# Kernel optimization log

Hardware: AMD Instinct MI355X
Metric: run time of the kernel (lower is better)

Reference implementation:

```python
import jax, jax.numpy as jnp
import numpy as np

N = 100000
E = 3200000
IN_DIM = 256
HID = 64
OUT = 40


def setup_inputs() -> dict:
    key = jax.random.key(0)
    ks = jax.random.split(key, 8)
    x = jax.random.normal(ks[0], (N, IN_DIM), dtype=jnp.float32)
    edge_index = jax.random.randint(ks[1], (2, E), 0, N, dtype=jnp.int64)
    # Glorot-ish init for weights
    W1 = jax.random.normal(ks[2], (IN_DIM, HID), dtype=jnp.float32) / np.sqrt(IN_DIM)
    b1 = jnp.zeros((HID,), dtype=jnp.float32)
    W2 = jax.random.normal(ks[3], (HID, HID), dtype=jnp.float32) / np.sqrt(HID)
    b2 = jnp.zeros((HID,), dtype=jnp.float32)
    W3 = jax.random.normal(ks[4], (HID, OUT), dtype=jnp.float32) / np.sqrt(HID)
    b3 = jax.random.normal(ks[5], (OUT,), dtype=jnp.float32) * 0.01
    return {"x": x, "edge_index": edge_index,
            "W1": W1, "b1": b1, "W2": W2, "b2": b2, "W3": W3, "b3": b3}


def _gcn_norm(edge_index, n):
    # Add self-loops, compute symmetric normalization deg^-1/2 A deg^-1/2
    loop = jnp.arange(n, dtype=edge_index.dtype)
    src = jnp.concatenate([edge_index[0], loop])
    dst = jnp.concatenate([edge_index[1], loop])
    deg = jax.ops.segment_sum(jnp.ones_like(dst, dtype=jnp.float32), dst,
                              num_segments=n)
    dinv = jnp.where(deg > 0, jax.lax.rsqrt(deg), 0.0)
    norm = dinv[src] * dinv[dst]  # [E+N]
    return src, dst, norm


def _gcn_conv(x, src, dst, norm, W, b, n):
    h = x @ W                                  # transform first (small dim)
    msg = h[src] * norm[:, None]               # gather + scale
    out = jax.ops.segment_sum(msg, dst, num_segments=n)  # scatter-add
    return out + b


def reference(x, edge_index, W1, b1, W2, b2, W3, b3):
    n = x.shape[0]
    src, dst, norm = _gcn_norm(edge_index, n)
    h = jax.nn.relu(_gcn_conv(x, src, dst, norm, W1, b1, n))
    h = jax.nn.relu(_gcn_conv(h, src, dst, norm, W2, b2, n))
    logits = h @ W3 + b3
    return jax.nn.log_softmax(logits, axis=1)
```

## Files before the change

kernel.cpp:

```cpp
#include <hip/hip_runtime.h>
#include <hip/hip_fp16.h>
#include <cstdint>


constexpr int CHUNK = 8192;
constexpr int BKCAP = 8192;

typedef __attribute__((ext_vector_type(8))) short bf16x8;
typedef __attribute__((ext_vector_type(4))) float f32x4;

__device__ __forceinline__ int cvt2bf(float a, float b) {
    int r;
    asm("v_cvt_pk_bf16_f32 %0, %1, %2" : "=v"(r) : "v"(a), "v"(b));
    return r;
}
__device__ __forceinline__ unsigned short bf16_1(float a) {
    return (unsigned short)(cvt2bf(a, a) & 0xFFFF);
}

__global__ __launch_bounds__(256) void p2_localsort(
        const int* __restrict__ esrc, const int* __restrict__ edst, int E,
        unsigned* __restrict__ pairs1, int* __restrict__ cntMat,
        int* __restrict__ startMat, int NBK) {
    __shared__ int hist[1024];
    __shared__ int wsum[256];
    __shared__ unsigned lp[CHUNK];
    const int t = threadIdx.x, blk = blockIdx.x;
    const int base = blk * CHUNK;
    const int cnt = min(CHUNK, E - base);
    for (int i = t; i < 1024; i += 256) hist[i] = 0;
    __syncthreads();
    for (int i = t; i < cnt; i += 256) atomicAdd(&hist[edst[base + i] >> 7], 1);
    __syncthreads();
    int h0 = hist[4*t], h1 = hist[4*t+1], h2 = hist[4*t+2], h3 = hist[4*t+3];
    int s = h0 + h1 + h2 + h3;
    wsum[t] = s; __syncthreads();
    #pragma unroll
    for (int o = 1; o < 256; o <<= 1) {
        int x = (t >= o) ? wsum[t - o] : 0;
        __syncthreads(); wsum[t] += x; __syncthreads();
    }
    int run = wsum[t] - s;
    int e0 = run, e1 = run + h0, e2 = e1 + h1, e3 = e2 + h2;
    hist[4*t] = e0; hist[4*t+1] = e1; hist[4*t+2] = e2; hist[4*t+3] = e3;
    if (4*t     < NBK) { cntMat[(size_t)blk*NBK + 4*t]     = h0; startMat[(size_t)blk*NBK + 4*t]     = e0; }
    if (4*t + 1 < NBK) { cntMat[(size_t)blk*NBK + 4*t + 1] = h1; startMat[(size_t)blk*NBK + 4*t + 1] = e1; }
    if (4*t + 2 < NBK) { cntMat[(size_t)blk*NBK + 4*t + 2] = h2; startMat[(size_t)blk*NBK + 4*t + 2] = e2; }
    if (4*t + 3 < NBK) { cntMat[(size_t)blk*NBK + 4*t + 3] = h3; startMat[(size_t)blk*NBK + 4*t + 3] = e3; }
    __syncthreads();
    for (int i = t; i < cnt; i += 256) {
        int d = edst[base + i];
        int pos = atomicAdd(&hist[d >> 7], 1);
        lp[pos] = ((unsigned)(d & 127) << 17) | (unsigned)esrc[base + i];
    }
    __syncthreads();
    for (int i = t; i < cnt; i += 256) pairs1[base + i] = lp[i];
}

__global__ __launch_bounds__(256) void p3_colscan(int* __restrict__ cntMat,
        int* __restrict__ TB, int nchunks, int NBK) {
    __shared__ int buf[512];
    const int t = threadIdx.x, b = blockIdx.x;
    int v0 = (t < nchunks) ? cntMat[(size_t)t*NBK + b] : 0;
    int v1 = (t + 256 < nchunks) ? cntMat[(size_t)(t + 256)*NBK + b] : 0;
    buf[t] = v0; buf[t + 256] = v1; __syncthreads();
    #pragma unroll
    for (int o = 1; o < 512; o <<= 1) {
        int x0 = (t >= o) ? buf[t - o] : 0;
        int x1 = (t + 256 >= o) ? buf[t + 256 - o] : 0;
        __syncthreads(); buf[t] += x0; buf[t + 256] += x1; __syncthreads();
    }
    if (t < nchunks) cntMat[(size_t)t*NBK + b] = buf[t] - v0;
    if (t + 256 < nchunks) cntMat[(size_t)(t + 256)*NBK + b] = buf[t + 256] - v1;
    if (t == 0) TB[b] = buf[511];
}

__global__ __launch_bounds__(256) void p4_scan(const int* __restrict__ TB,
        int* __restrict__ bucketBase, int NBK, int E) {
    __shared__ int buf[1024];
    __shared__ int wsum[256];
    const int t = threadIdx.x;
    for (int i = t; i < 1024; i += 256) buf[i] = (i < NBK) ? TB[i] : 0;
    __syncthreads();
    int h0 = buf[4*t], h1 = buf[4*t+1], h2 = buf[4*t+2], h3 = buf[4*t+3];
    int s = h0 + h1 + h2 + h3;
    wsum[t] = s; __syncthreads();
    #pragma unroll
    for (int o = 1; o < 256; o <<= 1) {
        int x = (t >= o) ? wsum[t - o] : 0;
        __syncthreads(); wsum[t] += x; __syncthreads();
    }
    int run = wsum[t] - s;
    int e0 = run, e1 = run + h0, e2 = e1 + h1, e3 = e2 + h2;
    if (4*t     < NBK) bucketBase[4*t]     = e0;
    if (4*t + 1 < NBK) bucketBase[4*t + 1] = e1;
    if (4*t + 2 < NBK) bucketBase[4*t + 2] = e2;
    if (4*t + 3 < NBK) bucketBase[4*t + 3] = e3;
    if (t == 0) bucketBase[NBK] = E;
}

__global__ __launch_bounds__(256) void p6_sortcsr(
        const unsigned* __restrict__ pairs1, const int* __restrict__ cumMat,
        const int* __restrict__ startMat, const int* __restrict__ TB,
        const int* __restrict__ bucketBase, int nchunks, int NBK,
        int* __restrict__ csrc, int* __restrict__ rofs,
        float* __restrict__ dinv, int N, int E) {
    __shared__ unsigned lp[BKCAP];
    __shared__ int ccum[512];
    __shared__ int cstart[512];
    __shared__ int hist[128];
    __shared__ int sc[128];
    __shared__ int foffs[128];
    const int t = threadIdx.x, b = blockIdx.x;
    const int total0 = TB[b];
    const int total = min(total0, BKCAP);
    const int base = bucketBase[b];
    for (int i = t; i < nchunks; i += 256) {
        ccum[i]   = cumMat[(size_t)i * NBK + b];
        cstart[i] = startMat[(size_t)i * NBK + b];
    }
    if (t < 128) hist[t] = 0;
    if (t == 0) ccum[nchunks] = total0;
    __syncthreads();
    for (int i = t; i < total; i += 256) {
        int lo = 0, hi = nchunks - 1;
        while (lo < hi) {
            int mid = (lo + hi + 1) >> 1;
            if (ccum[mid] <= i) lo = mid; else hi = mid - 1;
        }
        unsigned v = pairs1[(size_t)lo * CHUNK + cstart[lo] + (i - ccum[lo])];
        lp[i] = v;
        atomicAdd(&hist[v >> 17], 1);
    }
    __syncthreads();
    if (t < 128) sc[t] = hist[t];
    __syncthreads();
    #pragma unroll
    for (int o = 1; o < 128; o <<= 1) {
        int x = (t >= o && t < 128) ? sc[t - o] : 0;
        __syncthreads();
        if (t < 128) sc[t] += x;
        __syncthreads();
    }
    if (t < 128) {
        int excl = sc[t] - hist[t];
        foffs[t] = excl;
        int node = b * 128 + t;
        if (node < N) {
            rofs[node] = base + excl;
            dinv[node] = rsqrtf((float)hist[t] + 1.0f);
        }
    }
    if (b == 0 && t == 255) rofs[N] = E;
    __syncthreads();
    for (int i = t; i < total; i += 256) {
        unsigned v = lp[i];
        int pos = atomicAdd(&foffs[v >> 17], 1);
        csrc[base + pos] = (int)(v & 0x1FFFFu);
    }
}

template<int K>
__global__ __launch_bounds__(256) void k_gemm(const float* __restrict__ X,
        const float* __restrict__ Wm, const float* __restrict__ dinv,
        __half* __restrict__ G, int nrows) {
    constexpr int BK = 32;
    constexpr int NCH = K / BK;
    constexpr int XP = 68;
    __shared__ float Xs[BK * XP];
    __shared__ float Ws[BK * 64];
    const int t = threadIdx.x;
    const int cg = t & 15;
    const int rg = t >> 4;
    const int brow = blockIdx.x * 64;

    float acc[4][4];
    #pragma unroll
    for (int r = 0; r < 4; ++r)
        #pragma unroll
        for (int c = 0; c < 4; ++c) acc[r][c] = 0.f;

    for (int ch = 0; ch < NCH; ++ch) {
        if (ch) __syncthreads();
        #pragma unroll
        for (int i = 0; i < 2; ++i) {
            int f = t + i * 256;
            int r = f >> 3, c4 = f & 7;
            int gr = brow + r;
            float4 v = make_float4(0.f, 0.f, 0.f, 0.f);
            if (gr < nrows)
                v = *(const float4*)(X + (size_t)gr * K + ch * BK + c4 * 4);
            int rsw = r ^ (c4 << 2);
            Xs[(c4 * 4 + 0) * XP + rsw] = v.x;
            Xs[(c4 * 4 + 1) * XP + rsw] = v.y;
            Xs[(c4 * 4 + 2) * XP + rsw] = v.z;
            Xs[(c4 * 4 + 3) * XP + rsw] = v.w;
        }
        #pragma unroll
        for (int i = 0; i < 2; ++i) {
            int f = t + i * 256;
            int k = f >> 4, c4 = f & 15;
            *(float4*)(Ws + k * 64 + c4 * 4) =
                *(const float4*)(Wm + (size_t)(ch * BK + k) * 64 + c4 * 4);
        }
        __syncthreads();

        #pragma unroll
        for (int k = 0; k < BK; ++k) {
            const int xsw = (k >> 2) << 2;
            float4 xa = *(const float4*)(Xs + k * XP + ((rg * 4) ^ xsw));
            float4 wv = *(const float4*)(Ws + k * 64 + cg * 4);
            acc[0][0] += xa.x * wv.x; acc[0][1] += xa.x * wv.y;
            acc[0][2] += xa.x * wv.z; acc[0][3] += xa.x * wv.w;
            acc[1][0] += xa.y * wv.x; acc[1][1] += xa.y * wv.y;
            acc[1][2] += xa.y * wv.z; acc[1][3] += xa.y * wv.w;
            acc[2][0] += xa.z * wv.x; acc[2][1] += xa.z * wv.y;
            acc[2][2] += xa.z * wv.z; acc[2][3] += xa.z * wv.w;
            acc[3][0] += xa.w * wv.x; acc[3][1] += xa.w * wv.y;
            acc[3][2] += xa.w * wv.z; acc[3][3] += xa.w * wv.w;
        }
    }
    #pragma unroll
    for (int r = 0; r < 4; ++r) {
        int gr = brow + rg * 4 + r;
        if (gr < nrows) {
            float dv = dinv[gr];
            __half2 h01 = __floats2half2_rn(acc[r][0] * dv, acc[r][1] * dv);
            __half2 h23 = __floats2half2_rn(acc[r][2] * dv, acc[r][3] * dv);
            uint2 pk;
            pk.x = *(unsigned*)&h01; pk.y = *(unsigned*)&h23;
            *(uint2*)(G + (size_t)gr * 64 + cg * 4) = pk;
        }
    }
}

#define ACC8H(HA, V) { \
    HA[0] = __hadd2(HA[0], *(const __half2*)&(V).x); \
    HA[1] = __hadd2(HA[1], *(const __half2*)&(V).y); \
    HA[2] = __hadd2(HA[2], *(const __half2*)&(V).z); \
    HA[3] = __hadd2(HA[3], *(const __half2*)&(V).w); }

#define GATHER_REDUCE(G_, beg_, end_, g_, p_, HA) { \
    int e = (beg_) + (g_); \
    for (; e + 8 < (end_); e += 16) { \
        int s0 = csrc[e]; \
        int s1 = csrc[e + 8]; \
        uint4 v0 = *(const uint4*)((G_) + (size_t)s0 * 64 + (p_) * 8); \
        uint4 v1 = *(const uint4*)((G_) + (size_t)s1 * 64 + (p_) * 8); \
        ACC8H(HA, v0) \
        ACC8H(HA, v1) \
    } \
    if (e < (end_)) { \
        int s = csrc[e]; \
        uint4 v = *(const uint4*)((G_) + (size_t)s * 64 + (p_) * 8); \
        ACC8H(HA, v) \
    } \
    _Pragma("unroll") \
    for (int off = 8; off <= 32; off <<= 1) { \
        _Pragma("unroll") \
        for (int q = 0; q < 4; ++q) { \
            int o = __shfl_xor(*(int*)&HA[q], off); \
            HA[q] = __hadd2(HA[q], *(__half2*)&o); \
        } \
    } }

#define CONV_EPILOGUE(G_, d_, dv_, bias_, p_, HA, HOUT) { \
    uint4 sv = *(const uint4*)((G_) + (size_t)(d_) * 64 + (p_) * 8); \
    float4 bb0 = *(const float4*)((bias_) + (p_) * 8); \
    float4 bb1 = *(const float4*)((bias_) + (p_) * 8 + 4); \
    float2 a0 = __half22float2(HA[0]), a1 = __half22float2(HA[1]); \
    float2 a2 = __half22float2(HA[2]), a3 = __half22float2(HA[3]); \
    float2 s0 = __half22float2(*(const __half2*)&sv.x); \
    float2 s1 = __half22float2(*(const __half2*)&sv.y); \
    float2 s2 = __half22float2(*(const __half2*)&sv.z); \
    float2 s3 = __half22float2(*(const __half2*)&sv.w); \
    HOUT[0] = fmaxf((a0.x + s0.x) * (dv_) + bb0.x, 0.f); \
    HOUT[1] = fmaxf((a0.y + s0.y) * (dv_) + bb0.y, 0.f); \
    HOUT[2] = fmaxf((a1.x + s1.x) * (dv_) + bb0.z, 0.f); \
    HOUT[3] = fmaxf((a1.y + s1.y) * (dv_) + bb0.w, 0.f); \
    HOUT[4] = fmaxf((a2.x + s2.x) * (dv_) + bb1.x, 0.f); \
    HOUT[5] = fmaxf((a2.y + s2.y) * (dv_) + bb1.y, 0.f); \
    HOUT[6] = fmaxf((a3.x + s3.x) * (dv_) + bb1.z, 0.f); \
    HOUT[7] = fmaxf((a3.y + s3.y) * (dv_) + bb1.w, 0.f); }

__global__ __launch_bounds__(256) void k_agg_mid(const __half* __restrict__ G,
        const int* __restrict__ rofs, const int* __restrict__ csrc,
        const float* __restrict__ dinv, const float* __restrict__ b1,
        const float* __restrict__ W2, __half* __restrict__ G2, int nrows) {
    __shared__ unsigned short W2t[64 * 68];
    __shared__ unsigned short H1s[16 * 68];
    const int t = threadIdx.x;
    for (int i = t; i < 4096; i += 256) {
        int k = i >> 6, c = i & 63;
        W2t[c * 68 + k] = bf16_1(W2[i]);
    }
    const int l = t & 63;
    const int w = t >> 6;
    const int g = l >> 3, p = l & 7;
    const int nbase = blockIdx.x * 16;
    #pragma unroll 1
    for (int i = 0; i < 4; ++i) {
        int row = w * 4 + i;
        int d = nbase + row;
        if (d < nrows) {
            int beg = rofs[d], end = rofs[d + 1];
            __half2 ha[4];
            #pragma unroll
            for (int q = 0; q < 4; ++q) ha[q] = __half2(__float2half(0.f), __float2half(0.f));
            GATHER_REDUCE(G, beg, end, g, p, ha)
            float dv = dinv[d];
            float h1[8];
            CONV_EPILOGUE(G, d, dv, b1, p, ha, h1)
            if (g == 0) {
                int4 pk;
                pk.x = cvt2bf(h1[0], h1[1]); pk.y = cvt2bf(h1[2], h1[3]);
                pk.z = cvt2bf(h1[4], h1[5]); pk.w = cvt2bf(h1[6], h1[7]);
                *(int4*)(&H1s[row * 68 + p * 8]) = pk;
            }
        }
    }
    __syncthreads();
    const int c16 = l & 15, g4 = l >> 4;
    f32x4 acc = {0.f, 0.f, 0.f, 0.f};
    #pragma unroll
    for (int kc = 0; kc < 2; ++kc) {
        bf16x8 a = *(bf16x8*)(&H1s[c16 * 68 + kc * 32 + g4 * 8]);
        bf16x8 b = *(bf16x8*)(&W2t[(w * 16 + c16) * 68 + kc * 32 + g4 * 8]);
        acc = __builtin_amdgcn_mfma_f32_16x16x32_bf16(a, b, acc, 0, 0, 0);
    }
    #pragma unroll
    for (int r = 0; r < 4; ++r) {
        int d = nbase + g4 * 4 + r;
        if (d < nrows)
            G2[(size_t)d * 64 + w * 16 + c16] = __float2half(acc[r] * dinv[d]);
    }
}

__global__ __launch_bounds__(256) void k_agg_out(const __half* __restrict__ G2,
        const int* __restrict__ rofs, const int* __restrict__ csrc,
        const float* __restrict__ dinv, const float* __restrict__ b2,
        const float* __restrict__ W3, const float* __restrict__ b3,
        float* __restrict__ out, int nrows) {
    constexpr int LP = 49;
    __shared__ unsigned short W3t[48 * 68];
    __shared__ unsigned short H2s[16 * 68];
    __shared__ float Ls[16 * LP];
    __shared__ float b3s[48];
    const int t = threadIdx.x;
    for (int i = t; i < 48 * 64; i += 256) {
        int c = i >> 6, k = i & 63;
        W3t[c * 68 + k] = (c < 40) ? bf16_1(W3[k * 40 + c]) : (unsigned short)0;
    }
    if (t < 48) b3s[t] = (t < 40) ? b3[t] : 0.f;
    const int l = t & 63;
    const int w = t >> 6;
    const int g = l >> 3, p = l & 7;
    const int nbase = blockIdx.x * 16;
    #pragma unroll 1
    for (int i = 0; i < 4; ++i) {
        int row = w * 4 + i;
        int d = nbase + row;
        if (d < nrows) {
            int beg = rofs[d], end = rofs[d + 1];
            __half2 ha[4];
            #pragma unroll
            for (int q = 0; q < 4; ++q) ha[q] = __half2(__float2half(0.f), __float2half(0.f));
            GATHER_REDUCE(G2, beg, end, g, p, ha)
            float dv = dinv[d];
            float h2[8];
            CONV_EPILOGUE(G2, d, dv, b2, p, ha, h2)
            if (g == 0) {
                int4 pk;
                pk.x = cvt2bf(h2[0], h2[1]); pk.y = cvt2bf(h2[2], h2[3]);
                pk.z = cvt2bf(h2[4], h2[5]); pk.w = cvt2bf(h2[6], h2[7]);
                *(int4*)(&H2s[row * 68 + p * 8]) = pk;
            }
        }
    }
    __syncthreads();
    const int c16 = l & 15, g4 = l >> 4;
    if (w < 3) {
        f32x4 acc = {0.f, 0.f, 0.f, 0.f};
        #pragma unroll
        for (int kc = 0; kc < 2; ++kc) {
            bf16x8 a = *(bf16x8*)(&H2s[c16 * 68 + kc * 32 + g4 * 8]);
            bf16x8 b = *(bf16x8*)(&W3t[(w * 16 + c16) * 68 + kc * 32 + g4 * 8]);
            acc = __builtin_amdgcn_mfma_f32_16x16x32_bf16(a, b, acc, 0, 0, 0);
        }
        #pragma unroll
        for (int r = 0; r < 4; ++r)
            Ls[(g4 * 4 + r) * LP + w * 16 + c16] = acc[r] + b3s[w * 16 + c16];
    }
    __syncthreads();
    #pragma unroll 1
    for (int i = 0; i < 4; ++i) {
        int row = w * 4 + i;
        int d = nbase + row;
        if (d >= nrows) continue;
        float v = (l < 40) ? Ls[row * LP + l] : -3.4e38f;
        float m = v;
        #pragma unroll
        for (int off = 1; off < 64; off <<= 1) m = fmaxf(m, __shfl_xor(m, off));
        float ex = (l < 40) ? expf(v - m) : 0.f;
        float ssum = ex;
        #pragma unroll
        for (int off = 1; off < 64; off <<= 1) ssum += __shfl_xor(ssum, off);
        float lse = m + logf(ssum);
        if (l < 40) out[(size_t)d * 40 + l] = v - lse;
    }
}

extern "C" void kernel_launch(void* const* d_in, const int* in_sizes, int n_in,
                              void* d_out, int out_size, void* d_ws, size_t ws_size,
                              hipStream_t stream) {
    const float* x  = (const float*)d_in[0];
    const int*   ei = (const int*)d_in[1];
    const float* W1 = (const float*)d_in[2];
    const float* b1 = (const float*)d_in[3];
    const float* W2 = (const float*)d_in[4];
    const float* b2 = (const float*)d_in[5];
    const float* W3 = (const float*)d_in[6];
    const float* b3 = (const float*)d_in[7];
    float* out = (float*)d_out;

    const int HID = in_sizes[3];
    const int IND = in_sizes[2] / HID;
    const int N   = in_sizes[0] / IND;
    const int E   = in_sizes[1] / 2;
    (void)HID; (void)n_in; (void)out_size; (void)ws_size;

    const int NBK     = (N + 127) >> 7;
    const int nchunks = (E + CHUNK - 1) / CHUNK;

    char* ws = (char*)d_ws;
    size_t off = 0;
    auto alloc = [&](size_t bytes) -> char* {
        char* p = ws + off;
        off = (off + bytes + 255) & ~(size_t)255;
        return p;
    };
    size_t gbytes = (size_t)N * 64 * 2;
    size_t p1bytes = (size_t)E * 4;
    int*      cntMat     = (int*)     alloc((size_t)nchunks * NBK * 4);
    int*      startMat   = (int*)     alloc((size_t)nchunks * NBK * 4);
    int*      TB         = (int*)     alloc((size_t)NBK * 4);
    int*      bucketBase = (int*)     alloc(((size_t)NBK + 1) * 4);
    float*    dinv       = (float*)   alloc((size_t)N * 4);
    int*      rofs       = (int*)     alloc(((size_t)N + 1) * 4);
    int*      csrc       = (int*)     alloc((size_t)E * 4);
    __half*   g          = (__half*)  alloc(gbytes > p1bytes ? gbytes : p1bytes);
    __half*   g2         = (__half*)  alloc(gbytes);
    unsigned* pairs1     = (unsigned*)g;

    const int* esrc = ei;
    const int* edst = ei + E;
    const int gM  = (N + 63) / 64;
    const int gA  = (N + 15) / 16;

    p2_localsort<<<nchunks, 256, 0, stream>>>(esrc, edst, E, pairs1, cntMat, startMat, NBK);
    p3_colscan  <<<NBK, 256, 0, stream>>>(cntMat, TB, nchunks, NBK);
    p4_scan     <<<1, 256, 0, stream>>>(TB, bucketBase, NBK, E);
    p6_sortcsr  <<<NBK, 256, 0, stream>>>(pairs1, cntMat, startMat, TB, bucketBase,
                                          nchunks, NBK, csrc, rofs, dinv, N, E);

    k_gemm<256> <<<gM, 256, 0, stream>>>(x, W1, dinv, g, N);
    k_agg_mid   <<<gA, 256, 0, stream>>>(g, rofs, csrc, dinv, b1, W2, g2, N);
    k_agg_out   <<<gA, 256, 0, stream>>>(g2, rofs, csrc, dinv, b2, W3, b3, out, N);
}
```

Before: 300.6 us.

## Process four destination rows per wavefront concurrently in aggregation kernels

Changes the aggregation mapping so that each wavefront handles four destination rows at once, with 16 lanes per row split into two edge-slices of eight feature lanes. Before, each wavefront looped serially over its four rows with eight edge-slices per row. The gather loop is unrolled to four outstanding 16-byte loads per lane, and the cross-lane reduction shrinks to a single shuffle. The aim is more memory-level parallelism and fewer serial latency chains per row, at the cost of divergence when the four rows have uneven degrees.

New measurement: 277.0 us. 7.9% less time.

```diff
diff --git a/kernel.cpp b/kernel.cpp
--- a/kernel.cpp
+++ b/kernel.cpp
@@ -240,28 +240,25 @@
     HA[2] = __hadd2(HA[2], *(const __half2*)&(V).z); \
     HA[3] = __hadd2(HA[3], *(const __half2*)&(V).w); }
 
-#define GATHER_REDUCE(G_, beg_, end_, g_, p_, HA) { \
-    int e = (beg_) + (g_); \
-    for (; e + 8 < (end_); e += 16) { \
-        int s0 = csrc[e]; \
-        int s1 = csrc[e + 8]; \
-        uint4 v0 = *(const uint4*)((G_) + (size_t)s0 * 64 + (p_) * 8); \
-        uint4 v1 = *(const uint4*)((G_) + (size_t)s1 * 64 + (p_) * 8); \
-        ACC8H(HA, v0) \
-        ACC8H(HA, v1) \
+#define GATHER16(G_, beg_, end_, s_, p_, HA) { \
+    int e = (beg_) + (s_); \
+    for (; e + 6 < (end_); e += 8) { \
+        int i0 = csrc[e], i1 = csrc[e + 2], i2 = csrc[e + 4], i3 = csrc[e + 6]; \
+        uint4 v0 = *(const uint4*)((G_) + (size_t)i0 * 64 + (p_) * 8); \
+        uint4 v1 = *(const uint4*)((G_) + (size_t)i1 * 64 + (p_) * 8); \
+        uint4 v2 = *(const uint4*)((G_) + (size_t)i2 * 64 + (p_) * 8); \
+        uint4 v3 = *(const uint4*)((G_) + (size_t)i3 * 64 + (p_) * 8); \
+        ACC8H(HA, v0) ACC8H(HA, v1) ACC8H(HA, v2) ACC8H(HA, v3) \
     } \
-    if (e < (end_)) { \
-        int s = csrc[e]; \
-        uint4 v = *(const uint4*)((G_) + (size_t)s * 64 + (p_) * 8); \
+    for (; e < (end_); e += 2) { \
+        int ii = csrc[e]; \
+        uint4 v = *(const uint4*)((G_) + (size_t)ii * 64 + (p_) * 8); \
         ACC8H(HA, v) \
     } \
     _Pragma("unroll") \
-    for (int off = 8; off <= 32; off <<= 1) { \
-        _Pragma("unroll") \
-        for (int q = 0; q < 4; ++q) { \
-            int o = __shfl_xor(*(int*)&HA[q], off); \
-            HA[q] = __hadd2(HA[q], *(__half2*)&o); \
-        } \
+    for (int q = 0; q < 4; ++q) { \
+        int o = __shfl_xor(*(int*)&HA[q], 8); \
+        HA[q] = __hadd2(HA[q], *(__half2*)&o); \
     } }
 
 #define CONV_EPILOGUE(G_, d_, dv_, bias_, p_, HA, HOUT) { \
@@ -296,31 +293,30 @@
     }
     const int l = t & 63;
     const int w = t >> 6;
-    const int g = l >> 3, p = l & 7;
+    const int n = l >> 4;
+    const int s = (l >> 3) & 1;
+    const int p = l & 7;
+    const int row = w * 4 + n;
+    const int d = blockIdx.x * 16 + row;
+    if (d < nrows) {
+        const int beg = rofs[d], end = rofs[d + 1];
+        __half2 ha[4];
+        #pragma unroll
+        for (int q = 0; q < 4; ++q) ha[q] = __half2(__float2half(0.f), __float2half(0.f));
+        GATHER16(G, beg, end, s, p, ha)
+        float dv = dinv[d];
+        float h1[8];
+        CONV_EPILOGUE(G, d, dv, b1, p, ha, h1)
+        if (s == 0) {
+            int4 pk;
+            pk.x = cvt2bf(h1[0], h1[1]); pk.y = cvt2bf(h1[2], h1[3]);
+            pk.z = cvt2bf(h1[4], h1[5]); pk.w = cvt2bf(h1[6], h1[7]);
+            *(int4*)(&H1s[row * 68 + p * 8]) = pk;
+        }
+    }
+    __syncthreads();
+    const int c16 = l & 15, g4 = l >> 4;
     const int nbase = blockIdx.x * 16;
-    #pragma unroll 1
-    for (int i = 0; i < 4; ++i) {
-        int row = w * 4 + i;
-        int d = nbase + row;
-        if (d < nrows) {
-            int beg = rofs[d], end = rofs[d + 1];
-            __half2 ha[4];
-            #pragma unroll
-            for (int q = 0; q < 4; ++q) ha[q] = __half2(__float2half(0.f), __float2half(0.f));
-            GATHER_REDUCE(G, beg, end, g, p, ha)
-            float dv = dinv[d];
-            float h1[8];
-            CONV_EPILOGUE(G, d, dv, b1, p, ha, h1)
-            if (g == 0) {
-                int4 pk;
-                pk.x = cvt2bf(h1[0], h1[1]); pk.y = cvt2bf(h1[2], h1[3]);
-                pk.z = cvt2bf(h1[4], h1[5]); pk.w = cvt2bf(h1[6], h1[7]);
-                *(int4*)(&H1s[row * 68 + p * 8]) = pk;
-            }
-        }
-    }
-    __syncthreads();
-    const int c16 = l & 15, g4 = l >> 4;
     f32x4 acc = {0.f, 0.f, 0.f, 0.f};
     #pragma unroll
     for (int kc = 0; kc < 2; ++kc) {
@@ -330,9 +326,9 @@
     }
     #pragma unroll
     for (int r = 0; r < 4; ++r) {
-        int d = nbase + g4 * 4 + r;
-        if (d < nrows)
-            G2[(size_t)d * 64 + w * 16 + c16] = __float2half(acc[r] * dinv[d]);
+        int dd = nbase + g4 * 4 + r;
+        if (dd < nrows)
+            G2[(size_t)dd * 64 + w * 16 + c16] = __float2half(acc[r] * dinv[dd]);
     }
 }
 
@@ -354,31 +350,30 @@
     if (t < 48) b3s[t] = (t < 40) ? b3[t] : 0.f;
     const int l = t & 63;
     const int w = t >> 6;
-    const int g = l >> 3, p = l & 7;
+    const int n = l >> 4;
+    const int s = (l >> 3) & 1;
+    const int p = l & 7;
+    const int row = w * 4 + n;
+    const int d = blockIdx.x * 16 + row;
+    if (d < nrows) {
+        const int beg = rofs[d], end = rofs[d + 1];
+        __half2 ha[4];
+        #pragma unroll
+        for (int q = 0; q < 4; ++q) ha[q] = __half2(__float2half(0.f), __float2half(0.f));
+        GATHER16(G2, beg, end, s, p, ha)
+        float dv = dinv[d];
+        float h2[8];
+        CONV_EPILOGUE(G2, d, dv, b2, p, ha, h2)
+        if (s == 0) {
+            int4 pk;
+            pk.x = cvt2bf(h2[0], h2[1]); pk.y = cvt2bf(h2[2], h2[3]);
+            pk.z = cvt2bf(h2[4], h2[5]); pk.w = cvt2bf(h2[6], h2[7]);
+            *(int4*)(&H2s[row * 68 + p * 8]) = pk;
+        }
+    }
+    __syncthreads();
+    const int c16 = l & 15, g4 = l >> 4;
     const int nbase = blockIdx.x * 16;
-    #pragma unroll 1
-    for (int i = 0; i < 4; ++i) {
-        int row = w * 4 + i;
-        int d = nbase + row;
-        if (d < nrows) {
-            int beg = rofs[d], end = rofs[d + 1];
-            __half2 ha[4];
-            #pragma unroll
-            for (int q = 0; q < 4; ++q) ha[q] = __half2(__float2half(0.f), __float2half(0.f));
-            GATHER_REDUCE(G2, beg, end, g, p, ha)
-            float dv = dinv[d];
-            float h2[8];
-            CONV_EPILOGUE(G2, d, dv, b2, p, ha, h2)
-            if (g == 0) {
-                int4 pk;
-                pk.x = cvt2bf(h2[0], h2[1]); pk.y = cvt2bf(h2[2], h2[3]);
-                pk.z = cvt2bf(h2[4], h2[5]); pk.w = cvt2bf(h2[6], h2[7]);
-                *(int4*)(&H2s[row * 68 + p * 8]) = pk;
-            }
-        }
-    }
-    __syncthreads();
-    const int c16 = l & 15, g4 = l >> 4;
     if (w < 3) {
         f32x4 acc = {0.f, 0.f, 0.f, 0.f};
         #pragma unroll
@@ -394,10 +389,10 @@
     __syncthreads();
     #pragma unroll 1
     for (int i = 0; i < 4; ++i) {
-        int row = w * 4 + i;
-        int d = nbase + row;
-        if (d >= nrows) continue;
-        float v = (l < 40) ? Ls[row * LP + l] : -3.4e38f;
+        int rr = w * 4 + i;
+        int dd = nbase + rr;
+        if (dd >= nrows) continue;
+        float v = (l < 40) ? Ls[rr * LP + l] : -3.4e38f;
         float m = v;
         #pragma unroll
         for (int off = 1; off < 64; off <<= 1) m = fmaxf(m, __shfl_xor(m, off));
@@ -406,7 +401,7 @@
         #pragma unroll
         for (int off = 1; off < 64; off <<= 1) ssum += __shfl_xor(ssum, off);
         float lse = m + logf(ssum);
-        if (l < 40) out[(size_t)d * 40 + l] = v - lse;
+        if (l < 40) out[(size_t)dd * 40 + l] = v - lse;
     }
 }
 
```

## Give each wave its own row in aggregation kernels to drop block barriers

Applied to the files above, without the earlier changes.

The two aggregation kernels are restructured so that each wave gathers one destination row, then runs its own MFMA on that row. This removes the block-wide barrier between the gather and the matmul, so waves with short neighbour lists no longer wait for slower ones. The weights are staged into shared memory already in MFMA fragment layout, and log-softmax is done with 16-lane shuffles straight from the accumulators, so the logits no longer go through shared memory. The trade-off is four times as many blocks, each re-converting the full weight matrix into shared memory. Each MFMA now also produces only one useful row out of sixteen.

After: 402.0 us. 1.34x slower.

```diff
diff --git a/kernel.cpp b/kernel.cpp
--- a/kernel.cpp
+++ b/kernel.cpp
@@ -283,56 +283,60 @@
     HOUT[6] = fmaxf((a3.x + s3.x) * (dv_) + bb1.z, 0.f); \
     HOUT[7] = fmaxf((a3.y + s3.y) * (dv_) + bb1.w, 0.f); }
 
+#define STORE_ROW0(HT, HOUT, l_, p_) { \
+    if ((l_) < 8) { \
+        int4 pk; \
+        pk.x = cvt2bf(HOUT[0], HOUT[1]); pk.y = cvt2bf(HOUT[2], HOUT[3]); \
+        pk.z = cvt2bf(HOUT[4], HOUT[5]); pk.w = cvt2bf(HOUT[6], HOUT[7]); \
+        *(int4*)(&(HT)[(p_) * 8]) = pk; \
+    } \
+    asm volatile("" ::: "memory"); }
+
 __global__ __launch_bounds__(256) void k_agg_mid(const __half* __restrict__ G,
         const int* __restrict__ rofs, const int* __restrict__ csrc,
         const float* __restrict__ dinv, const float* __restrict__ b1,
         const float* __restrict__ W2, __half* __restrict__ G2, int nrows) {
-    __shared__ unsigned short W2t[64 * 68];
-    __shared__ unsigned short H1s[16 * 68];
+    __shared__ __attribute__((aligned(16))) unsigned short Wf[8 * 64 * 8];
+    __shared__ __attribute__((aligned(16))) unsigned short Ht[4 * 16 * 68];
     const int t = threadIdx.x;
-    for (int i = t; i < 4096; i += 256) {
-        int k = i >> 6, c = i & 63;
-        W2t[c * 68 + k] = bf16_1(W2[i]);
-    }
+    for (int idx = t; idx < 4096; idx += 256) {
+        int f = idx >> 9, ln = (idx >> 3) & 63, j = idx & 7;
+        int kc = f & 1, ct = f >> 1;
+        int k = kc * 32 + ((ln >> 4) << 3) + j;
+        int c = ct * 16 + (ln & 15);
+        Wf[idx] = bf16_1(W2[k * 64 + c]);
+    }
+    __syncthreads();
     const int l = t & 63;
     const int w = t >> 6;
     const int g = l >> 3, p = l & 7;
-    const int nbase = blockIdx.x * 16;
-    #pragma unroll 1
-    for (int i = 0; i < 4; ++i) {
-        int row = w * 4 + i;
-        int d = nbase + row;
-        if (d < nrows) {
-            int beg = rofs[d], end = rofs[d + 1];
-            __half2 ha[4];
-            #pragma unroll
-            for (int q = 0; q < 4; ++q) ha[q] = __half2(__float2half(0.f), __float2half(0.f));
-            GATHER_REDUCE(G, beg, end, g, p, ha)
-            float dv = dinv[d];
-            float h1[8];
-            CONV_EPILOGUE(G, d, dv, b1, p, ha, h1)
-            if (g == 0) {
-                int4 pk;
-                pk.x = cvt2bf(h1[0], h1[1]); pk.y = cvt2bf(h1[2], h1[3]);
-                pk.z = cvt2bf(h1[4], h1[5]); pk.w = cvt2bf(h1[6], h1[7]);
-                *(int4*)(&H1s[row * 68 + p * 8]) = pk;
-            }
-        }
-    }
-    __syncthreads();
+    const int d = blockIdx.x * 4 + w;
+    if (d >= nrows) return;
+    const int beg = rofs[d], end = rofs[d + 1];
+    __half2 ha[4];
+    #pragma unroll
+    for (int q = 0; q < 4; ++q) ha[q] = __half2(__float2half(0.f), __float2half(0.f));
+    GATHER_REDUCE(G, beg, end, g, p, ha)
+    const float dv = dinv[d];
+    float h1[8];
+    CONV_EPILOGUE(G, d, dv, b1, p, ha, h1)
+    unsigned short* Hw = &Ht[w * (16 * 68)];
+    STORE_ROW0(Hw, h1, l, p)
     const int c16 = l & 15, g4 = l >> 4;
-    f32x4 acc = {0.f, 0.f, 0.f, 0.f};
+    f32x4 acc[4] = {{0,0,0,0},{0,0,0,0},{0,0,0,0},{0,0,0,0}};
     #pragma unroll
     for (int kc = 0; kc < 2; ++kc) {
-        bf16x8 a = *(bf16x8*)(&H1s[c16 * 68 + kc * 32 + g4 * 8]);
-        bf16x8 b = *(bf16x8*)(&W2t[(w * 16 + c16) * 68 + kc * 32 + g4 * 8]);
-        acc = __builtin_amdgcn_mfma_f32_16x16x32_bf16(a, b, acc, 0, 0, 0);
-    }
-    #pragma unroll
-    for (int r = 0; r < 4; ++r) {
-        int d = nbase + g4 * 4 + r;
-        if (d < nrows)
-            G2[(size_t)d * 64 + w * 16 + c16] = __float2half(acc[r] * dinv[d]);
+        bf16x8 a = *(bf16x8*)(&Hw[c16 * 68 + kc * 32 + g4 * 8]);
+        #pragma unroll
+        for (int ct = 0; ct < 4; ++ct) {
+            bf16x8 b = *(bf16x8*)(&Wf[(ct * 2 + kc) * 512 + l * 8]);
+            acc[ct] = __builtin_amdgcn_mfma_f32_16x16x32_bf16(a, b, acc[ct], 0, 0, 0);
+        }
+    }
+    if (l < 16) {
+        #pragma unroll
+        for (int ct = 0; ct < 4; ++ct)
+            G2[(size_t)d * 64 + ct * 16 + l] = __float2half(acc[ct][0] * dv);
     }
 }
 
@@ -341,72 +345,57 @@
         const float* __restrict__ dinv, const float* __restrict__ b2,
         const float* __restrict__ W3, const float* __restrict__ b3,
         float* __restrict__ out, int nrows) {
-    constexpr int LP = 49;
-    __shared__ unsigned short W3t[48 * 68];
-    __shared__ unsigned short H2s[16 * 68];
-    __shared__ float Ls[16 * LP];
-    __shared__ float b3s[48];
+    __shared__ __attribute__((aligned(16))) unsigned short Wf[6 * 64 * 8];
+    __shared__ __attribute__((aligned(16))) unsigned short Ht[4 * 16 * 68];
     const int t = threadIdx.x;
-    for (int i = t; i < 48 * 64; i += 256) {
-        int c = i >> 6, k = i & 63;
-        W3t[c * 68 + k] = (c < 40) ? bf16_1(W3[k * 40 + c]) : (unsigned short)0;
-    }
-    if (t < 48) b3s[t] = (t < 40) ? b3[t] : 0.f;
+    for (int idx = t; idx < 3072; idx += 256) {
+        int f = idx >> 9, ln = (idx >> 3) & 63, j = idx & 7;
+        int kc = f & 1, ct = f >> 1;
+        int k = kc * 32 + ((ln >> 4) << 3) + j;
+        int c = ct * 16 + (ln & 15);
+        Wf[idx] = (c < 40) ? bf16_1(W3[k * 40 + c]) : (unsigned short)0;
+    }
+    __syncthreads();
     const int l = t & 63;
     const int w = t >> 6;
     const int g = l >> 3, p = l & 7;
-    const int nbase = blockIdx.x * 16;
-    #pragma unroll 1
-    for (int i = 0; i < 4; ++i) {
-        int row = w * 4 + i;
-        int d = nbase + row;
-        if (d < nrows) {
-            int beg = rofs[d], end = rofs[d + 1];
-            __half2 ha[4];
-            #pragma unroll
-            for (int q = 0; q < 4; ++q) ha[q] = __half2(__float2half(0.f), __float2half(0.f));
-            GATHER_REDUCE(G2, beg, end, g, p, ha)
-            float dv = dinv[d];
-            float h2[8];
-            CONV_EPILOGUE(G2, d, dv, b2, p, ha, h2)
-            if (g == 0) {
-                int4 pk;
-                pk.x = cvt2bf(h2[0], h2[1]); pk.y = cvt2bf(h2[2], h2[3]);
-                pk.z = cvt2bf(h2[4], h2[5]); pk.w = cvt2bf(h2[6], h2[7]);
-                *(int4*)(&H2s[row * 68 + p * 8]) = pk;
-            }
-        }
-    }
-    __syncthreads();
+    const int d = blockIdx.x * 4 + w;
+    if (d >= nrows) return;
+    const int beg = rofs[d], end = rofs[d + 1];
+    __half2 ha[4];
+    #pragma unroll
+    for (int q = 0; q < 4; ++q) ha[q] = __half2(__float2half(0.f), __float2half(0.f));
+    GATHER_REDUCE(G2, beg, end, g, p, ha)
+    const float dv = dinv[d];
+    float h2[8];
+    CONV_EPILOGUE(G2, d, dv, b2, p, ha, h2)
+    unsigned short* Hw = &Ht[w * (16 * 68)];
+    STORE_ROW0(Hw, h2, l, p)
     const int c16 = l & 15, g4 = l >> 4;
-    if (w < 3) {
-        f32x4 acc = {0.f, 0.f, 0.f, 0.f};
-        #pragma unroll
-        for (int kc = 0; kc < 2; ++kc) {
-            bf16x8 a = *(bf16x8*)(&H2s[c16 * 68 + kc * 32 + g4 * 8]);
-            bf16x8 b = *(bf16x8*)(&W3t[(w * 16 + c16) * 68 + kc * 32 + g4 * 8]);
-            acc = __builtin_amdgcn_mfma_f32_16x16x32_bf16(a, b, acc, 0, 0, 0);
-        }
-        #pragma unroll
-        for (int r = 0; r < 4; ++r)
-            Ls[(g4 * 4 + r) * LP + w * 16 + c16] = acc[r] + b3s[w * 16 + c16];
-    }
-    __syncthreads();
-    #pragma unroll 1
-    for (int i = 0; i < 4; ++i) {
-        int row = w * 4 + i;
-        int d = nbase + row;
-        if (d >= nrows) continue;
-        float v = (l < 40) ? Ls[row * LP + l] : -3.4e38f;
-        float m = v;
-        #pragma unroll
-        for (int off = 1; off < 64; off <<= 1) m = fmaxf(m, __shfl_xor(m, off));
-        float ex = (l < 40) ? expf(v - m) : 0.f;
-        float ssum = ex;
-        #pragma unroll
-        for (int off = 1; off < 64; off <<= 1) ssum += __shfl_xor(ssum, off);
-        float lse = m + logf(ssum);
-        if (l < 40) out[(size_t)d * 40 + l] = v - lse;
+    f32x4 acc[3] = {{0,0,0,0},{0,0,0,0},{0,0,0,0}};
+    #pragma unroll
+    for (int kc = 0; kc < 2; ++kc) {
+        bf16x8 a = *(bf16x8*)(&Hw[c16 * 68 + kc * 32 + g4 * 8]);
+        #pragma unroll
+        for (int ct = 0; ct < 3; ++ct) {
+            bf16x8 b = *(bf16x8*)(&Wf[(ct * 2 + kc) * 512 + l * 8]);
+            acc[ct] = __builtin_amdgcn_mfma_f32_16x16x32_bf16(a, b, acc[ct], 0, 0, 0);
+        }
+    }
+    float L0 = acc[0][0] + b3[c16];
+    float L1 = acc[1][0] + b3[16 + c16];
+    float L2 = (c16 < 8) ? acc[2][0] + b3[32 + (c16 & 7)] : -3.4e38f;
+    float m = fmaxf(fmaxf(L0, L1), L2);
+    #pragma unroll
+    for (int off = 1; off <= 8; off <<= 1) m = fmaxf(m, __shfl_xor(m, off));
+    float ssum = expf(L0 - m) + expf(L1 - m) + ((c16 < 8) ? expf(L2 - m) : 0.f);
+    #pragma unroll
+    for (int off = 1; off <= 8; off <<= 1) ssum += __shfl_xor(ssum, off);
+    float lse = m + logf(ssum);
+    if (l < 16) {
+        out[(size_t)d * 40 + l] = L0 - lse;
+        out[(size_t)d * 40 + 16 + l] = L1 - lse;
+        if (l < 8) out[(size_t)d * 40 + 32 + l] = L2 - lse;
     }
 }
 
@@ -455,7 +444,7 @@
     const int* esrc = ei;
     const int* edst = ei + E;
     const int gM  = (N + 63) / 64;
-    const int gA  = (N + 15) / 16;
+    const int gA  = (N + 3) / 4;
 
     p2_localsort<<<nchunks, 256, 0, stream>>>(esrc, edst, E, pairs1, cntMat, startMat, NBK);
     p3_colscan  <<<NBK, 256, 0, stream>>>(cntMat, TB, nchunks, NBK);
```
